# Kernel tuning notes

Hardware: AMD Instinct MI355X
Metric: run time of the kernel (lower is better)

Reference implementation:

```python
import jax, jax.numpy as jnp
import numpy as np

B, L, H = 32, 512, 1024
MAX_HEADERS = 32   # static cap on header runs per sample (torch version is dynamic)
MAX_HLEN = 12      # static cap on tokens per header run


def setup_inputs() -> dict:
    key = jax.random.key(0)
    enc = jax.random.normal(key, (B, L, H), dtype=jnp.float32)
    # Structured segments matching the code's semantics: 0=pad, 1=header run,
    # 2=question token (out[s==2]), 3=separator.
    rng = np.random.default_rng(0)
    seg = np.zeros((B, L), dtype=np.int32)
    for b in range(B):
        lq = int(rng.integers(32, 96))
        seg[b, :lq] = 2
        pos = lq
        nh = int(rng.integers(4, MAX_HEADERS))
        for _ in range(nh):
            hl = int(rng.integers(1, MAX_HLEN))
            if pos + hl + 1 >= L:
                break
            seg[b, pos:pos + hl] = 1
            pos += hl
            seg[b, pos] = 3  # separator ends the run
            pos += 1
    return {"encoder_output": enc, "segment": jnp.asarray(seg)}


def _unpack(enc, seg):
    # enc: [B,L,H], seg: [B,L]
    Lloc = enc.shape[1]
    ar = jnp.arange(Lloc)
    # ---- question tokens (seg==2), gathered in order, zero-padded to L ----
    q_mask = seg == 2                                        # [B,L]
    sort_key = jnp.where(q_mask, ar[None, :], Lloc + ar[None, :])
    order = jnp.argsort(sort_key, axis=1)                    # question positions first, in order
    q_gather = jnp.take_along_axis(enc, order[:, :, None], axis=1)
    q_valid = jnp.take_along_axis(q_mask, order, axis=1)
    question_hidden = q_gather * q_valid[:, :, None].astype(enc.dtype)  # [B,L,H]
    # ---- header runs: maximal contiguous stretches of seg==1 ----
    is_h = seg == 1
    prev = jnp.pad(is_h[:, :-1], ((0, 0), (1, 0)))
    run_start = is_h & ~prev                                  # first token of each run
    run_id = jnp.cumsum(run_start.astype(jnp.int32), axis=1) - 1
    last_start = jax.lax.cummax(jnp.where(run_start, ar[None, :], -1), axis=1)
    pos_in_run = ar[None, :] - last_start                     # offset within current run
    valid = is_h & (pos_in_run < MAX_HLEN) & (run_id < MAX_HEADERS)
    hid = jnp.where(valid, run_id, MAX_HEADERS)               # invalid tokens -> dump row
    pid = jnp.clip(pos_in_run, 0, MAX_HLEN - 1)
    buf = jnp.zeros((enc.shape[0], MAX_HEADERS + 1, MAX_HLEN, H), enc.dtype)
    bidx = jnp.arange(enc.shape[0])[:, None]
    buf = buf.at[bidx, hid, pid].set(enc)                     # batched scatter of header tokens
    headers = buf[:, :MAX_HEADERS]                            # [B,MAX_HEADERS,MAX_HLEN,H]
    return question_hidden, headers


def reference(encoder_output, segment):
    return _unpack(encoder_output, segment)
```

## Files before the change

### kernel.cpp

```cpp
#include <hip/hip_runtime.h>

#define BB 32
#define LL 512
#define HH 1024
#define MAXH 32
#define MAXHL 12
#define HROWS (MAXH * MAXHL)

__global__ __launch_bounds__(64) void meta_kernel(const int* __restrict__ seg,
                                                  int* __restrict__ src_q,
                                                  int* __restrict__ src_h) {
    __shared__ int lq[LL];
    __shared__ int lh[HROWS];
    const int b = blockIdx.x;
    const int t = threadIdx.x;

    for (int k = t; k < LL; k += 64) lq[k] = -1;
    for (int k = t; k < HROWS; k += 64) lh[k] = -1;
    __syncthreads();

    int s[8];
    const int base = b * LL + t * 8;
#pragma unroll
    for (int k = 0; k < 8; ++k) s[k] = seg[base + k];

    int last_ish = (s[7] == 1) ? 1 : 0;
    int prev_from_left = __shfl_up(last_ish, 1);
    if (t == 0) prev_from_left = 0;

    int qc = 0, rc = 0, mstart = -1;
    {
        int ph = prev_from_left;
#pragma unroll
        for (int k = 0; k < 8; ++k) {
            int ish = (s[k] == 1);
            if (s[k] == 2) qc++;
            if (ish && !ph) { rc++; mstart = t * 8 + k; }
            ph = ish;
        }
    }

    int iq = qc, ir = rc, im = mstart;
    for (int off = 1; off < 64; off <<= 1) {
        int uq = __shfl_up(iq, off);
        int ur = __shfl_up(ir, off);
        int um = __shfl_up(im, off);
        if (t >= off) {
            iq += uq;
            ir += ur;
            im = max(im, um);
        }
    }
    int exq = iq - qc;
    int exr = ir - rc;
    int exm = __shfl_up(im, 1);
    if (t == 0) exm = -1;

    {
        int qpos = exq, runs = exr, last = exm, ph = prev_from_left;
#pragma unroll
        for (int k = 0; k < 8; ++k) {
            int i = t * 8 + k;
            int ish = (s[k] == 1);
            if (ish && !ph) { runs++; last = i; }
            if (ish) {
                int pos = i - last;
                int rid = runs - 1;
                if (pos < MAXHL && rid < MAXH) lh[rid * MAXHL + pos] = i;
            }
            if (s[k] == 2) { lq[qpos] = i; qpos++; }
            ph = ish;
        }
    }
    __syncthreads();

    for (int k = t; k < LL; k += 64) src_q[b * LL + k] = lq[k];
    for (int k = t; k < HROWS; k += 64) src_h[b * HROWS + k] = lh[k];
}

__global__ __launch_bounds__(256) void copy_kernel(const float* __restrict__ enc,
                                                   const int* __restrict__ src_q,
                                                   const int* __restrict__ src_h,
                                                   float* __restrict__ out) {
    const int bid = blockIdx.x;
    const int t = threadIdx.x;

    int b, src;
    long long outOff;
    if (bid < BB * LL) {
        b = bid >> 9;
        src = src_q[bid];
        outOff = (long long)bid * HH;
    } else {
        int hb = bid - BB * LL;
        b = hb / HROWS;
        src = src_h[hb];
        outOff = (long long)BB * LL * HH + (long long)hb * HH;
    }

    float4* dst = reinterpret_cast<float4*>(out + outOff) + t;
    if (src >= 0) {
        const float4* sp =
            reinterpret_cast<const float4*>(enc + ((long long)(b * LL + src)) * HH) + t;
        *dst = *sp;
    } else {
        *dst = make_float4(0.f, 0.f, 0.f, 0.f);
    }
}

extern "C" void kernel_launch(void* const* d_in, const int* in_sizes, int n_in,
                              void* d_out, int out_size, void* d_ws, size_t ws_size,
                              hipStream_t stream) {
    const float* enc = (const float*)d_in[0];
    const int* seg = (const int*)d_in[1];
    float* out = (float*)d_out;

    int* src_q = (int*)d_ws;
    int* src_h = src_q + BB * LL;

    meta_kernel<<<BB, 64, 0, stream>>>(seg, src_q, src_h);
    copy_kernel<<<BB * LL + BB * HROWS, 256, 0, stream>>>(enc, src_q, src_h, out);
}
```

Baseline: 28.74 us.

## Fuse index computation into copy kernel, recomputing scans per block of four rows

```diff
diff --git a/kernel.cpp b/kernel.cpp
--- a/kernel.cpp
+++ b/kernel.cpp
@@ -6,105 +6,113 @@
 #define MAXH 32
 #define MAXHL 12
 #define HROWS (MAXH * MAXHL)
+#define RPB 4
 
-__global__ __launch_bounds__(64) void meta_kernel(const int* __restrict__ seg,
-                                                  int* __restrict__ src_q,
-                                                  int* __restrict__ src_h) {
-    __shared__ int lq[LL];
-    __shared__ int lh[HROWS];
-    const int b = blockIdx.x;
+#define NQG (LL / RPB)
+#define NHG (HROWS / RPB)
+#define QBLOCKS (BB * NQG)
+#define HBLOCKS (BB * NHG)
+
+__global__ __launch_bounds__(256) void fused_kernel(const float* __restrict__ enc,
+                                                    const int* __restrict__ seg,
+                                                    float* __restrict__ out) {
+    __shared__ int s_src[RPB];
+    const int bid = blockIdx.x;
     const int t = threadIdx.x;
 
-    for (int k = t; k < LL; k += 64) lq[k] = -1;
-    for (int k = t; k < HROWS; k += 64) lh[k] = -1;
-    __syncthreads();
-
-    int s[8];
-    const int base = b * LL + t * 8;
-#pragma unroll
-    for (int k = 0; k < 8; ++k) s[k] = seg[base + k];
-
-    int last_ish = (s[7] == 1) ? 1 : 0;
-    int prev_from_left = __shfl_up(last_ish, 1);
-    if (t == 0) prev_from_left = 0;
-
-    int qc = 0, rc = 0, mstart = -1;
-    {
-        int ph = prev_from_left;
-#pragma unroll
-        for (int k = 0; k < 8; ++k) {
-            int ish = (s[k] == 1);
-            if (s[k] == 2) qc++;
-            if (ish && !ph) { rc++; mstart = t * 8 + k; }
-            ph = ish;
-        }
+    int b, qmode, idx0;
+    long long outRow0;
+    if (bid < QBLOCKS) {
+        b = bid >> 7;
+        idx0 = (bid & (NQG - 1)) * RPB;
+        qmode = 1;
+        outRow0 = (long long)b * LL + idx0;
+    } else {
+        int hb = bid - QBLOCKS;
+        b = hb / NHG;
+        idx0 = (hb % NHG) * RPB;
+        qmode = 0;
+        outRow0 = (long long)BB * LL + (long long)b * HROWS + idx0;
     }
 
-    int iq = qc, ir = rc, im = mstart;
-    for (int off = 1; off < 64; off <<= 1) {
-        int uq = __shfl_up(iq, off);
-        int ur = __shfl_up(ir, off);
-        int um = __shfl_up(im, off);
-        if (t >= off) {
-            iq += uq;
-            ir += ur;
-            im = max(im, um);
+    if (t < 64) {
+        if (t < RPB) s_src[t] = -1;
+        int s[8];
+        const int base = b * LL + t * 8;
+#pragma unroll
+        for (int k = 0; k < 8; ++k) s[k] = seg[base + k];
+
+        int last_ish = (s[7] == 1) ? 1 : 0;
+        int prev_from_left = __shfl_up(last_ish, 1);
+        if (t == 0) prev_from_left = 0;
+
+        int qc = 0, rc = 0, mstart = -1;
+        {
+            int ph = prev_from_left;
+#pragma unroll
+            for (int k = 0; k < 8; ++k) {
+                int ish = (s[k] == 1);
+                if (s[k] == 2) qc++;
+                if (ish && !ph) { rc++; mstart = t * 8 + k; }
+                ph = ish;
+            }
         }
-    }
-    int exq = iq - qc;
-    int exr = ir - rc;
-    int exm = __shfl_up(im, 1);
-    if (t == 0) exm = -1;
 
-    {
-        int qpos = exq, runs = exr, last = exm, ph = prev_from_left;
+        int iq = qc, ir = rc, im = mstart;
 #pragma unroll
-        for (int k = 0; k < 8; ++k) {
-            int i = t * 8 + k;
-            int ish = (s[k] == 1);
-            if (ish && !ph) { runs++; last = i; }
-            if (ish) {
-                int pos = i - last;
-                int rid = runs - 1;
-                if (pos < MAXHL && rid < MAXH) lh[rid * MAXHL + pos] = i;
+        for (int off = 1; off < 64; off <<= 1) {
+            int uq = __shfl_up(iq, off);
+            int ur = __shfl_up(ir, off);
+            int um = __shfl_up(im, off);
+            if (t >= off) {
+                iq += uq;
+                ir += ur;
+                im = max(im, um);
             }
-            if (s[k] == 2) { lq[qpos] = i; qpos++; }
-            ph = ish;
+        }
+        int exq = iq - qc;
+        int exr = ir - rc;
+        int exm = __shfl_up(im, 1);
+        if (t == 0) exm = -1;
+
+        {
+            int qpos = exq, runs = exr, last = exm, ph = prev_from_left;
+#pragma unroll
+            for (int k = 0; k < 8; ++k) {
+                int i = t * 8 + k;
+                int ish = (s[k] == 1);
+                if (ish && !ph) { runs++; last = i; }
+                if (qmode) {
+                    if (s[k] == 2) {
+                        int d = qpos - idx0;
+                        if (d >= 0 && d < RPB) s_src[d] = i;
+                        qpos++;
+                    }
+                } else if (ish) {
+                    int pos = i - last;
+                    int rid = runs - 1;
+                    if (pos < MAXHL && rid < MAXH) {
+                        int d = rid * MAXHL + pos - idx0;
+                        if (d >= 0 && d < RPB) s_src[d] = i;
+                    }
+                }
+                ph = ish;
+            }
         }
     }
     __syncthreads();
 
-    for (int k = t; k < LL; k += 64) src_q[b * LL + k] = lq[k];
-    for (int k = t; k < HROWS; k += 64) src_h[b * HROWS + k] = lh[k];
-}
-
-__global__ __launch_bounds__(256) void copy_kernel(const float* __restrict__ enc,
-                                                   const int* __restrict__ src_q,
-                                                   const int* __restrict__ src_h,
-                                                   float* __restrict__ out) {
-    const int bid = blockIdx.x;
-    const int t = threadIdx.x;
-
-    int b, src;
-    long long outOff;
-    if (bid < BB * LL) {
-        b = bid >> 9;
-        src = src_q[bid];
-        outOff = (long long)bid * HH;
-    } else {
-        int hb = bid - BB * LL;
-        b = hb / HROWS;
-        src = src_h[hb];
-        outOff = (long long)BB * LL * HH + (long long)hb * HH;
-    }
-
-    float4* dst = reinterpret_cast<float4*>(out + outOff) + t;
-    if (src >= 0) {
-        const float4* sp =
-            reinterpret_cast<const float4*>(enc + ((long long)(b * LL + src)) * HH) + t;
-        *dst = *sp;
-    } else {
-        *dst = make_float4(0.f, 0.f, 0.f, 0.f);
+    const long long encBase = (long long)b * LL * HH;
+#pragma unroll
+    for (int r = 0; r < RPB; ++r) {
+        int src = s_src[r];
+        float4* dst = reinterpret_cast<float4*>(out + (outRow0 + r) * HH) + t;
+        if (src >= 0) {
+            const float4* sp = reinterpret_cast<const float4*>(enc + encBase + (long long)src * HH) + t;
+            *dst = *sp;
+        } else {
+            *dst = make_float4(0.f, 0.f, 0.f, 0.f);
+        }
     }
 }
 
@@ -114,10 +122,5 @@
     const float* enc = (const float*)d_in[0];
     const int* seg = (const int*)d_in[1];
     float* out = (float*)d_out;
-
-    int* src_q = (int*)d_ws;
-    int* src_h = src_q + BB * LL;
-
-    meta_kernel<<<BB, 64, 0, stream>>>(seg, src_q, src_h);
-    copy_kernel<<<BB * LL + BB * HROWS, 256, 0, stream>>>(enc, src_q, src_h, out);
+    fused_kernel<<<QBLOCKS + HBLOCKS, 256, 0, stream>>>(enc, seg, out);
 }
```

New measurement: 25.09 us. 12.7% less time.
